# Optimization experiments

Measured on AMD Instinct MI355X. Metric: run time of the kernel, lower is better.

Reference implementation:

```python
import jax, jax.numpy as jnp
import numpy as np

N = 50000
E_RAND = 800000
IN_CH = 128
HID = 64
HEADS = 4
OUT_CH = 3
NEG_SLOPE = 0.2
BN_EPS = 1e-5


def setup_inputs() -> dict:
    key = jax.random.key(0)
    ks = jax.random.split(key, 24)
    x = jax.random.normal(ks[0], (N, IN_CH), dtype=jnp.float32)
    er = jax.random.randint(ks[1], (2, E_RAND), 0, N)
    sl = jnp.tile(jnp.arange(N, dtype=er.dtype)[None, :], (2, 1))
    edge_index = jnp.concatenate([er, sl], axis=1)  # [2, 850000]
    s = 0.1
    d1 = HID * HEADS            # 256
    d2 = (HID // 2) * HEADS     # 128
    inp = dict(x=x, edge_index=edge_index)
    # layer 1: in 128 -> heads*64
    inp["W1"] = s * jax.random.normal(ks[2], (IN_CH, HEADS * HID), dtype=jnp.float32)
    inp["a1s"] = s * jax.random.normal(ks[3], (HEADS, HID), dtype=jnp.float32)
    inp["a1d"] = s * jax.random.normal(ks[4], (HEADS, HID), dtype=jnp.float32)
    inp["b1"] = jnp.zeros((d1,), jnp.float32)
    inp["g1"] = jnp.ones((d1,), jnp.float32)
    inp["be1"] = jnp.zeros((d1,), jnp.float32)
    inp["m1"] = 0.01 * jax.random.normal(ks[5], (d1,), dtype=jnp.float32)
    inp["v1"] = jnp.ones((d1,), jnp.float32) + 0.01 * jax.random.uniform(ks[6], (d1,))
    # layer 2: in 256 -> heads*32
    inp["W2"] = s * jax.random.normal(ks[7], (d1, HEADS * (HID // 2)), dtype=jnp.float32)
    inp["a2s"] = s * jax.random.normal(ks[8], (HEADS, HID // 2), dtype=jnp.float32)
    inp["a2d"] = s * jax.random.normal(ks[9], (HEADS, HID // 2), dtype=jnp.float32)
    inp["b2"] = jnp.zeros((d2,), jnp.float32)
    inp["g2"] = jnp.ones((d2,), jnp.float32)
    inp["be2"] = jnp.zeros((d2,), jnp.float32)
    inp["m2"] = 0.01 * jax.random.normal(ks[10], (d2,), dtype=jnp.float32)
    inp["v2"] = jnp.ones((d2,), jnp.float32) + 0.01 * jax.random.uniform(ks[11], (d2,))
    # layer 3: in 128 -> 1 head, out_ch, concat=False
    inp["W3"] = s * jax.random.normal(ks[12], (d2, OUT_CH), dtype=jnp.float32)
    inp["a3s"] = s * jax.random.normal(ks[13], (1, OUT_CH), dtype=jnp.float32)
    inp["a3d"] = s * jax.random.normal(ks[14], (1, OUT_CH), dtype=jnp.float32)
    inp["b3"] = jnp.zeros((OUT_CH,), jnp.float32)
    return inp


def gat_conv(x, src, dst, W, a_src, a_dst, b, heads, fdim, concat):
    n = x.shape[0]
    h = (x @ W).reshape(n, heads, fdim)           # [N,H,F]
    als = jnp.einsum('nhf,hf->nh', h, a_src)      # [N,H]
    ald = jnp.einsum('nhf,hf->nh', h, a_dst)
    e = jax.nn.leaky_relu(als[src] + ald[dst], NEG_SLOPE)  # [E,H]
    m = jax.lax.stop_gradient(jax.ops.segment_max(e, dst, num_segments=n))
    ex = jnp.exp(e - m[dst])
    ssum = jax.ops.segment_sum(ex, dst, num_segments=n)
    alpha = ex / (ssum[dst] + 1e-16)              # segment softmax over in-edges
    msg = h[src] * alpha[:, :, None]              # [E,H,F]
    out = jax.ops.segment_sum(msg, dst, num_segments=n)  # [N,H,F]
    out = out.reshape(n, heads * fdim) if concat else out.mean(axis=1)
    return out + b


def batch_norm(x, gamma, beta, mean, var):
    return (x - mean) * jax.lax.rsqrt(var + BN_EPS) * gamma + beta


def reference(x, edge_index, W1, a1s, a1d, b1, g1, be1, m1, v1,
              W2, a2s, a2d, b2, g2, be2, m2, v2,
              W3, a3s, a3d, b3):
    src, dst = edge_index[0], edge_index[1]
    h = gat_conv(x, src, dst, W1, a1s, a1d, b1, HEADS, HID, True)
    h = jax.nn.elu(batch_norm(h, g1, be1, m1, v1))
    h = gat_conv(h, src, dst, W2, a2s, a2d, b2, HEADS, HID // 2, True)
    h = jax.nn.elu(batch_norm(h, g2, be2, m2, v2))
    h = gat_conv(h, src, dst, W3, a3s, a3d, b3, 1, OUT_CH, False)
    return jax.nn.log_softmax(h, axis=1)
```

## Files before the change

### kernel.cpp

```cpp
#include <hip/hip_runtime.h>


#define WSZ 64

typedef short short8 __attribute__((ext_vector_type(8)));
typedef float float4v __attribute__((ext_vector_type(4)));

__device__ inline unsigned short f2bf(float f) {
  unsigned u = __float_as_uint(f);
  u += 0x7FFFu + ((u >> 16) & 1u);
  return (unsigned short)(u >> 16);
}


__global__ __launch_bounds__(256) void hist_kernel(const int* __restrict__ dst, int E,
                                                   int* __restrict__ deg) {
  int e = blockIdx.x * 256 + threadIdx.x;
  if (e < E) atomicAdd(&deg[dst[e]], 1);
}

__global__ __launch_bounds__(256) void block_sums_kernel(const int* __restrict__ deg, int n,
                                                         int* __restrict__ bsum) {
  __shared__ int sh[256];
  int t = threadIdx.x;
  int base = blockIdx.x * 1024 + t * 4;
  int v = 0;
#pragma unroll
  for (int j = 0; j < 4; ++j) {
    int idx = base + j;
    if (idx < n) v += deg[idx];
  }
  sh[t] = v;
  __syncthreads();
  for (int off = 128; off >= 1; off >>= 1) {
    if (t < off) sh[t] += sh[t + off];
    __syncthreads();
  }
  if (t == 0) bsum[blockIdx.x] = sh[0];
}

__global__ void tiny_scan_kernel(int* bsum, int nb) {
  if (threadIdx.x == 0 && blockIdx.x == 0) {
    int run = 0;
    for (int i = 0; i < nb; ++i) {
      int v = bsum[i];
      bsum[i] = run;
      run += v;
    }
  }
}

__global__ __launch_bounds__(256) void scan_write_kernel(const int* __restrict__ deg, int n,
                                                         const int* __restrict__ bbase,
                                                         int* __restrict__ row_start,
                                                         int* __restrict__ cursor) {
  __shared__ int sh[256];
  int t = threadIdx.x;
  int base = blockIdx.x * 1024 + t * 4;
  int v[4];
  int s = 0;
#pragma unroll
  for (int j = 0; j < 4; ++j) {
    int idx = base + j;
    v[j] = (idx < n) ? deg[idx] : 0;
    s += v[j];
  }
  sh[t] = s;
  __syncthreads();
  for (int off = 1; off < 256; off <<= 1) {
    int x = (t >= off) ? sh[t - off] : 0;
    __syncthreads();
    sh[t] += x;
    __syncthreads();
  }
  int excl = sh[t] - s + bbase[blockIdx.x];
#pragma unroll
  for (int j = 0; j < 4; ++j) {
    int idx = base + j;
    if (idx < n) {
      row_start[idx] = excl;
      cursor[idx] = excl;
    }
    excl += v[j];
  }
  if (blockIdx.x == gridDim.x - 1 && t == 255) row_start[n] = excl;
}

__global__ __launch_bounds__(256) void scatter_kernel(const int* __restrict__ src,
                                                      const int* __restrict__ dst, int E,
                                                      int* __restrict__ cursor,
                                                      int* __restrict__ csr_src) {
  int e = blockIdx.x * 256 + threadIdx.x;
  if (e < E) {
    int d = dst[e];
    int p = atomicAdd(&cursor[d], 1);
    csr_src[p] = src[e];
  }
}


__global__ __launch_bounds__(256) void conv_bf16x4(const float* __restrict__ in,
                                                   unsigned short* __restrict__ out, int n4) {
  int i = blockIdx.x * 256 + threadIdx.x;
  if (i < n4) {
    float4 v = ((const float4*)in)[i];
    ushort4 u;
    u.x = f2bf(v.x); u.y = f2bf(v.y); u.z = f2bf(v.z); u.w = f2bf(v.w);
    ((ushort4*)out)[i] = u;
  }
}

__global__ __launch_bounds__(256) void conv_w1t_kernel(const float* __restrict__ W1,
                                                       unsigned short* __restrict__ W1t) {
  int idx = blockIdx.x * 256 + threadIdx.x;
  int n = idx >> 7, k = idx & 127;
  W1t[idx] = f2bf(W1[k * 256 + n]);
}

__global__ __launch_bounds__(256) void conv_w2t_kernel(const float* __restrict__ W2,
                                                       unsigned short* __restrict__ W2t) {
  int idx = blockIdx.x * 256 + threadIdx.x;
  int n = idx >> 8, p = idx & 255;
  int kl = (p & ~63) | ((p & 3) << 4) | ((p >> 2) & 15);
  W2t[idx] = f2bf(W2[kl * 128 + n]);
}


template <int K, int NTOT>
__global__ __launch_bounds__(256) void gemm_mfma2(
    const unsigned short* __restrict__ A,
    const unsigned short* __restrict__ Bt,
    const float* __restrict__ a_s, const float* __restrict__ a_d,
    unsigned short* __restrict__ hout,
    float* __restrict__ als, float* __restrict__ ald,
    int M) {
  constexpr int COLS = NTOT / 2;
  constexpr int CFW = COLS / 16;
  constexpr int HLOG = NTOT / 4;
  constexpr int CFH = HLOG / 16;
  constexpr int VPT = NTOT / 64;
  constexpr int KS = K / 32;
  __shared__ __align__(16) unsigned short Bs[COLS][K + 8];

  const int t = threadIdx.x;
  const int w = t >> 6;
  const int lane = t & 63;
  const int c16 = lane & 15;
  const int q = lane >> 4;
  const int gcol = blockIdx.y;
  const int bm = blockIdx.x * 128;

  {
    constexpr int TPR = K / 64;
    int nloc = t / TPR;
    int part = (t % TPR) * 64;
    const unsigned short* srcp = Bt + (size_t)(gcol * COLS + nloc) * K + part;
#pragma unroll
    for (int j = 0; j < 8; ++j) {
      uint4 v = *(const uint4*)(srcp + j * 8);
      *(uint4*)&Bs[nloc][part + j * 8] = v;
    }
  }
  int arow[2];
  arow[0] = min(bm + w * 32 + c16, M - 1);
  arow[1] = min(bm + w * 32 + 16 + c16, M - 1);
  short8 afr[2];
#pragma unroll
  for (int rf = 0; rf < 2; ++rf)
    afr[rf] = *(const short8*)(A + (size_t)arow[rf] * K + q * 8);
  __syncthreads();

  float4v acc[2][CFW];
#pragma unroll
  for (int rf = 0; rf < 2; ++rf)
#pragma unroll
    for (int cf = 0; cf < CFW; ++cf) acc[rf][cf] = float4v{0.f, 0.f, 0.f, 0.f};

#pragma unroll
  for (int ks = 0; ks < KS; ++ks) {
    short8 anx[2];
    if (ks + 1 < KS) {
#pragma unroll
      for (int rf = 0; rf < 2; ++rf)
        anx[rf] = *(const short8*)(A + (size_t)arow[rf] * K + (ks + 1) * 32 + q * 8);
    }
#pragma unroll
    for (int cf = 0; cf < CFW; ++cf) {
      short8 bfrag = *(const short8*)&Bs[cf * 16 + c16][ks * 32 + q * 8];
#pragma unroll
      for (int rf = 0; rf < 2; ++rf)
        acc[rf][cf] =
            __builtin_amdgcn_mfma_f32_16x16x32_bf16(afr[rf], bfrag, acc[rf][cf], 0, 0, 0);
    }
    if (ks + 1 < KS) {
      afr[0] = anx[0];
      afr[1] = anx[1];
    }
  }

  float sasv[CFW], sadv[CFW];
#pragma unroll
  for (int cf = 0; cf < CFW; ++cf) {
    int L = gcol * COLS + cf * 16 + c16;
    sasv[cf] = a_s[L];
    sadv[cf] = a_d[L];
  }
#pragma unroll
  for (int rf = 0; rf < 2; ++rf) {
#pragma unroll
    for (int r = 0; r < 4; ++r) {
      int n = bm + w * 32 + rf * 16 + q * 4 + r;
      float ps[2] = {0.f, 0.f}, pd[2] = {0.f, 0.f};
      unsigned short us[CFW];
#pragma unroll
      for (int cf = 0; cf < CFW; ++cf) {
        float v = acc[rf][cf][r];
        us[cf] = f2bf(v);
        ps[cf / CFH] += v * sasv[cf];
        pd[cf / CFH] += v * sadv[cf];
      }
#pragma unroll
      for (int off = 1; off <= 8; off <<= 1) {
#pragma unroll
        for (int hl = 0; hl < 2; ++hl) {
          ps[hl] += __shfl_xor(ps[hl], off, 16);
          pd[hl] += __shfl_xor(pd[hl], off, 16);
        }
      }
      if (n < M) {
#pragma unroll
        for (int hl = 0; hl < 2; ++hl) {
          int head = gcol * 2 + hl;
          unsigned short* dst = hout + (size_t)n * NTOT + head * HLOG + c16 * VPT;
          if constexpr (VPT == 4) {
            ushort4 u;
            u.x = us[hl * 4 + 0]; u.y = us[hl * 4 + 1];
            u.z = us[hl * 4 + 2]; u.w = us[hl * 4 + 3];
            *(ushort4*)dst = u;
          } else {
            ushort2 u;
            u.x = us[hl * 2 + 0]; u.y = us[hl * 2 + 1];
            *(ushort2*)dst = u;
          }
          if (c16 == 0) {
            als[(size_t)n * 4 + head] = ps[hl];
            ald[(size_t)n * 4 + head] = pd[hl];
          }
        }
      }
    }
  }
}


template <int D, bool FUSEL3>
__global__ __launch_bounds__(256) void gat_aggregate(
    const unsigned short* __restrict__ h_bf, const float* __restrict__ als,
    const float* __restrict__ ald, const int* __restrict__ row_start,
    const int* __restrict__ csr_src, const float* __restrict__ bias,
    const float* __restrict__ gamma, const float* __restrict__ beta,
    const float* __restrict__ bmean, const float* __restrict__ bvar,
    unsigned short* __restrict__ obf,
    const float* __restrict__ W3, const float* __restrict__ a3s,
    const float* __restrict__ a3d, float4* __restrict__ h3p,
    float* __restrict__ ald3,
    int n_nodes) {
  constexpr int VPT = D / WSZ;
  constexpr int H = 4;
  __shared__ float w3s[384];
  __shared__ float sa3[6];
  if constexpr (FUSEL3) {
    for (int i = threadIdx.x; i < 384; i += 256) w3s[i] = W3[i];
    if (threadIdx.x < 3) {
      sa3[threadIdx.x] = a3s[threadIdx.x];
      sa3[3 + threadIdx.x] = a3d[threadIdx.x];
    }
    __syncthreads();
  }
  int wid = threadIdx.x >> 6, lane = threadIdx.x & 63;
  int n = blockIdx.x * 4 + wid;
  if (n >= n_nodes) return;
  int c = lane * VPT;
  int hd = lane >> 4;
  float aldv = ald[(size_t)n * H + hd];
  int row = row_start[n], end = row_start[n + 1];
  float acc[VPT] = {};
  float ssum = 0.f;
  int i = row;

#define EDGE_BLOCK(B)                                                          \
  for (; i + (B) - 1 < end; i += (B)) {                                        \
    int s[B];                                                                  \
    float e[B];                                                                \
    _Pragma("unroll") for (int j = 0; j < (B); ++j) s[j] = csr_src[i + j];     \
    _Pragma("unroll") for (int j = 0; j < (B); ++j) e[j] =                     \
        als[(size_t)s[j] * H + hd] + aldv;                                     \
    if constexpr (VPT == 4) {                                                  \
      uint2 u[B];                                                              \
      _Pragma("unroll") for (int j = 0; j < (B); ++j) u[j] =                   \
          *(const uint2*)(h_bf + (size_t)s[j] * D + c);                        \
      _Pragma("unroll") for (int j = 0; j < (B); ++j) {                        \
        float ee = e[j];                                                       \
        ee = (ee > 0.f) ? ee : 0.2f * ee;                                      \
        float ex = __expf(ee);                                                 \
        ssum += ex;                                                            \
        acc[0] += ex * __uint_as_float(u[j].x << 16);                          \
        acc[1] += ex * __uint_as_float(u[j].x & 0xFFFF0000u);                  \
        acc[2] += ex * __uint_as_float(u[j].y << 16);                          \
        acc[3] += ex * __uint_as_float(u[j].y & 0xFFFF0000u);                  \
      }                                                                        \
    } else {                                                                   \
      unsigned u[B];                                                           \
      _Pragma("unroll") for (int j = 0; j < (B); ++j) u[j] =                   \
          *(const unsigned*)(h_bf + (size_t)s[j] * D + c);                     \
      _Pragma("unroll") for (int j = 0; j < (B); ++j) {                        \
        float ee = e[j];                                                       \
        ee = (ee > 0.f) ? ee : 0.2f * ee;                                      \
        float ex = __expf(ee);                                                 \
        ssum += ex;                                                            \
        acc[0] += ex * __uint_as_float(u[j] << 16);                            \
        acc[1] += ex * __uint_as_float(u[j] & 0xFFFF0000u);                    \
      }                                                                        \
    }                                                                          \
  }

  EDGE_BLOCK(8)
  EDGE_BLOCK(4)
  EDGE_BLOCK(1)
#undef EDGE_BLOCK

  float inv = 1.f / (ssum + 1e-16f);
#pragma unroll
  for (int j = 0; j < VPT; ++j) {
    int cl = hd * (VPT * 16) + j * 16 + (lane & 15);
    float o = acc[j] * inv + bias[cl];
    o = (o - bmean[cl]) * rsqrtf(bvar[cl] + 1e-5f) * gamma[cl] + beta[cl];
    o = (o > 0.f) ? o : (__expf(o) - 1.f);
    acc[j] = o;
  }
  if constexpr (!FUSEL3) {
    ushort4 u;
    u.x = f2bf(acc[0]); u.y = f2bf(acc[1]); u.z = f2bf(acc[2]); u.w = f2bf(acc[3]);
    *(ushort4*)(obf + (size_t)n * D + c) = u;
  } else {
    int k0l = hd * 32 + (lane & 15);
    int k1l = k0l + 16;
    float p0 = acc[0] * w3s[k0l * 3 + 0] + acc[1] * w3s[k1l * 3 + 0];
    float p1 = acc[0] * w3s[k0l * 3 + 1] + acc[1] * w3s[k1l * 3 + 1];
    float p2 = acc[0] * w3s[k0l * 3 + 2] + acc[1] * w3s[k1l * 3 + 2];
#pragma unroll
    for (int off = 32; off >= 1; off >>= 1) {
      p0 += __shfl_xor(p0, off, 64);
      p1 += __shfl_xor(p1, off, 64);
      p2 += __shfl_xor(p2, off, 64);
    }
    if (lane == 0) {
      float als3 = p0 * sa3[0] + p1 * sa3[1] + p2 * sa3[2];
      float ad3 = p0 * sa3[3] + p1 * sa3[4] + p2 * sa3[5];
      h3p[n] = make_float4(p0, p1, p2, als3);
      ald3[n] = ad3;
    }
  }
}


__global__ __launch_bounds__(256) void l3_agg_kernel(const float4* __restrict__ h3p,
                                                     const float* __restrict__ ald3,
                                                     const int* __restrict__ row_start,
                                                     const int* __restrict__ csr_src,
                                                     const float* __restrict__ b3,
                                                     float* __restrict__ out, int n_nodes) {
  int wid = threadIdx.x >> 6, lane = threadIdx.x & 63;
  int n = blockIdx.x * 4 + wid;
  if (n >= n_nodes) return;
  float aldv = ald3[n];
  int row = row_start[n], end = row_start[n + 1];
  float a0 = 0.f, a1 = 0.f, a2 = 0.f, ss = 0.f;
  for (int i = row + lane; i < end; i += 64) {
    int s = csr_src[i];
    float4 hv = h3p[s];
    float e = hv.w + aldv;
    e = (e > 0.f) ? e : 0.2f * e;
    float ex = __expf(e);
    ss += ex;
    a0 += ex * hv.x;
    a1 += ex * hv.y;
    a2 += ex * hv.z;
  }
#pragma unroll
  for (int off = 32; off >= 1; off >>= 1) {
    a0 += __shfl_xor(a0, off, 64);
    a1 += __shfl_xor(a1, off, 64);
    a2 += __shfl_xor(a2, off, 64);
    ss += __shfl_xor(ss, off, 64);
  }
  if (lane == 0) {
    float inv = 1.f / (ss + 1e-16f);
    float o0 = a0 * inv + b3[0];
    float o1 = a1 * inv + b3[1];
    float o2 = a2 * inv + b3[2];
    float m = fmaxf(o0, fmaxf(o1, o2));
    float lse = m + logf(expf(o0 - m) + expf(o1 - m) + expf(o2 - m));
    out[n * 3 + 0] = o0 - lse;
    out[n * 3 + 1] = o1 - lse;
    out[n * 3 + 2] = o2 - lse;
  }
}


extern "C" void kernel_launch(void* const* d_in, const int* in_sizes, int n_in,
                              void* d_out, int out_size, void* d_ws, size_t ws_size,
                              hipStream_t stream) {
  const float* x   = (const float*)d_in[0];
  const int*   ei  = (const int*)d_in[1];
  const float* W1  = (const float*)d_in[2];
  const float* a1s = (const float*)d_in[3];
  const float* a1d = (const float*)d_in[4];
  const float* b1  = (const float*)d_in[5];
  const float* g1v = (const float*)d_in[6];
  const float* be1 = (const float*)d_in[7];
  const float* m1  = (const float*)d_in[8];
  const float* v1  = (const float*)d_in[9];
  const float* W2  = (const float*)d_in[10];
  const float* a2s = (const float*)d_in[11];
  const float* a2d = (const float*)d_in[12];
  const float* b2  = (const float*)d_in[13];
  const float* g2v = (const float*)d_in[14];
  const float* be2 = (const float*)d_in[15];
  const float* m2  = (const float*)d_in[16];
  const float* v2  = (const float*)d_in[17];
  const float* W3  = (const float*)d_in[18];
  const float* a3s = (const float*)d_in[19];
  const float* a3d = (const float*)d_in[20];
  const float* b3  = (const float*)d_in[21];
  float* out = (float*)d_out;

  const int N = in_sizes[0] / 128;
  const int E = in_sizes[1] / 2;
  const int* srcv = ei;
  const int* dstv = ei + E;

  float* wsf  = (float*)d_ws;
  float* als1 = wsf;
  float* ald1 = als1 + (size_t)N * 4;
  float* als2 = ald1 + (size_t)N * 4;
  float* ald2 = als2 + (size_t)N * 4;
  float* h3p  = ald2 + (size_t)N * 4;
  float* ald3 = h3p + (size_t)N * 4;
  unsigned short* x_bf  = (unsigned short*)(ald3 + N);
  unsigned short* h_bf1 = x_bf + (size_t)N * 128;
  unsigned short* o1_bf = h_bf1 + (size_t)N * 256;
  unsigned short* h_bf2 = o1_bf + (size_t)N * 256;
  unsigned short* W1t   = h_bf2 + (size_t)N * 128;
  unsigned short* W2t   = W1t + 256 * 128;
  int* deg       = (int*)(W2t + 128 * 256);
  int* row_start = deg + N;
  int* cursor    = row_start + (N + 1);
  int* csr_src   = cursor + (N + 1);
  int* bsum      = csr_src + E;

  const int eb = (E + 255) / 256;
  const int nb = (N + 1023) / 1024;
  const int nodes4 = (N + 3) / 4;
  const dim3 gemm_grid((N + 127) / 128, 2);

  conv_bf16x4<<<(N * 128 / 4 + 255) / 256, 256, 0, stream>>>(x, x_bf, N * 128 / 4);
  conv_w1t_kernel<<<128, 256, 0, stream>>>(W1, W1t);
  conv_w2t_kernel<<<128, 256, 0, stream>>>(W2, W2t);

  hipMemsetAsync(deg, 0, (size_t)N * sizeof(int), stream);
  hist_kernel<<<eb, 256, 0, stream>>>(dstv, E, deg);
  block_sums_kernel<<<nb, 256, 0, stream>>>(deg, N, bsum);
  tiny_scan_kernel<<<1, 64, 0, stream>>>(bsum, nb);
  scan_write_kernel<<<nb, 256, 0, stream>>>(deg, N, bsum, row_start, cursor);
  scatter_kernel<<<eb, 256, 0, stream>>>(srcv, dstv, E, cursor, csr_src);

  gemm_mfma2<128, 256><<<gemm_grid, 256, 0, stream>>>(x_bf, W1t, a1s, a1d, h_bf1, als1,
                                                      ald1, N);
  gat_aggregate<256, false><<<nodes4, 256, 0, stream>>>(
      h_bf1, als1, ald1, row_start, csr_src, b1, g1v, be1, m1, v1, o1_bf, nullptr, nullptr,
      nullptr, nullptr, nullptr, N);
  gemm_mfma2<256, 128><<<gemm_grid, 256, 0, stream>>>(o1_bf, W2t, a2s, a2d, h_bf2, als2,
                                                      ald2, N);
  gat_aggregate<128, true><<<nodes4, 256, 0, stream>>>(
      h_bf2, als2, ald2, row_start, csr_src, b2, g2v, be2, m2, v2, nullptr, W3, a3s, a3d,
      (float4*)h3p, ald3, N);
  l3_agg_kernel<<<nodes4, 256, 0, stream>>>((const float4*)h3p, ald3, row_start, csr_src,
                                            b3, out, N);
}
```

Before: 388.8 us.

## Fuse fp32-to-bf16 input conversion into first GEMM and merge small prep kernels

The first GEMM now reads fp32 x directly and converts it to bf16 in registers, so the separate conversion kernel and its bf16 buffer are gone. The two weight-transpose kernels are merged into one launch, and the serial block-sum scan becomes a wavefront shuffle scan. The GEMM also preloads all A fragments for every K step up front instead of double-buffering, which raises register pressure. Together these are meant to cut launches and one full pass over x, at the cost of the GEMM reading fp32 data, twice the bytes per A element. The shuffle scan only handles up to 64 blocks, which holds for N=50000.

```diff
diff --git a/kernel.cpp b/kernel.cpp
--- a/kernel.cpp
+++ b/kernel.cpp
@@ -39,15 +39,16 @@
   if (t == 0) bsum[blockIdx.x] = sh[0];
 }
 
-__global__ void tiny_scan_kernel(int* bsum, int nb) {
-  if (threadIdx.x == 0 && blockIdx.x == 0) {
-    int run = 0;
-    for (int i = 0; i < nb; ++i) {
-      int v = bsum[i];
-      bsum[i] = run;
-      run += v;
-    }
-  }
+__global__ void scan_blocks_kernel(int* bsum, int nb) {
+  int lane = threadIdx.x & 63;
+  int orig = (lane < nb) ? bsum[lane] : 0;
+  int v = orig;
+#pragma unroll
+  for (int off = 1; off < 64; off <<= 1) {
+    int o = __shfl_up(v, off, 64);
+    if (lane >= off) v += o;
+  }
+  if (lane < nb) bsum[lane] = v - orig;
 }
 
 __global__ __launch_bounds__(256) void scan_write_kernel(const int* __restrict__ deg, int n,
@@ -98,37 +99,27 @@
   }
 }
 
-
-__global__ __launch_bounds__(256) void conv_bf16x4(const float* __restrict__ in,
-                                                   unsigned short* __restrict__ out, int n4) {
-  int i = blockIdx.x * 256 + threadIdx.x;
-  if (i < n4) {
-    float4 v = ((const float4*)in)[i];
-    ushort4 u;
-    u.x = f2bf(v.x); u.y = f2bf(v.y); u.z = f2bf(v.z); u.w = f2bf(v.w);
-    ((ushort4*)out)[i] = u;
-  }
-}
-
-__global__ __launch_bounds__(256) void conv_w1t_kernel(const float* __restrict__ W1,
-                                                       unsigned short* __restrict__ W1t) {
-  int idx = blockIdx.x * 256 + threadIdx.x;
-  int n = idx >> 7, k = idx & 127;
-  W1t[idx] = f2bf(W1[k * 256 + n]);
-}
-
-__global__ __launch_bounds__(256) void conv_w2t_kernel(const float* __restrict__ W2,
-                                                       unsigned short* __restrict__ W2t) {
-  int idx = blockIdx.x * 256 + threadIdx.x;
-  int n = idx >> 8, p = idx & 255;
-  int kl = (p & ~63) | ((p & 3) << 4) | ((p >> 2) & 15);
-  W2t[idx] = f2bf(W2[kl * 128 + n]);
-}
-
-
-template <int K, int NTOT>
+__global__ __launch_bounds__(256) void conv_weights_kernel(const float* __restrict__ W1,
+                                                           const float* __restrict__ W2,
+                                                           unsigned short* __restrict__ W1t,
+                                                           unsigned short* __restrict__ W2t) {
+  int b = blockIdx.x;
+  if (b < 128) {
+    int idx = b * 256 + threadIdx.x;
+    int n = idx >> 7, k = idx & 127;
+    W1t[idx] = f2bf(W1[k * 256 + n]);
+  } else {
+    int idx = (b - 128) * 256 + threadIdx.x;
+    int n = idx >> 8, p = idx & 255;
+    int kl = (p & ~63) | ((p & 3) << 4) | ((p >> 2) & 15);
+    W2t[idx] = f2bf(W2[kl * 128 + n]);
+  }
+}
+
+
+template <int K, int NTOT, bool AF32>
 __global__ __launch_bounds__(256) void gemm_mfma2(
-    const unsigned short* __restrict__ A,
+    const void* __restrict__ Ap,
     const unsigned short* __restrict__ Bt,
     const float* __restrict__ a_s, const float* __restrict__ a_d,
     unsigned short* __restrict__ hout,
@@ -161,40 +152,60 @@
       *(uint4*)&Bs[nloc][part + j * 8] = v;
     }
   }
+
   int arow[2];
   arow[0] = min(bm + w * 32 + c16, M - 1);
   arow[1] = min(bm + w * 32 + 16 + c16, M - 1);
-  short8 afr[2];
+  short8 afr[2][KS];
+  if constexpr (AF32) {
+    float4 fv[2][KS][2];
+#pragma unroll
+    for (int rf = 0; rf < 2; ++rf) {
+      const float* rp = (const float*)Ap + (size_t)arow[rf] * K;
+#pragma unroll
+      for (int ks = 0; ks < KS; ++ks) {
+        fv[rf][ks][0] = *(const float4*)(rp + ks * 32 + q * 8);
+        fv[rf][ks][1] = *(const float4*)(rp + ks * 32 + q * 8 + 4);
+      }
+    }
+#pragma unroll
+    for (int rf = 0; rf < 2; ++rf)
+#pragma unroll
+      for (int ks = 0; ks < KS; ++ks) {
+        ushort4 u0, u1;
+        u0.x = f2bf(fv[rf][ks][0].x); u0.y = f2bf(fv[rf][ks][0].y);
+        u0.z = f2bf(fv[rf][ks][0].z); u0.w = f2bf(fv[rf][ks][0].w);
+        u1.x = f2bf(fv[rf][ks][1].x); u1.y = f2bf(fv[rf][ks][1].y);
+        u1.z = f2bf(fv[rf][ks][1].z); u1.w = f2bf(fv[rf][ks][1].w);
+        union { ushort4 u[2]; short8 s; } cvt;
+        cvt.u[0] = u0; cvt.u[1] = u1;
+        afr[rf][ks] = cvt.s;
+      }
+  } else {
+    const unsigned short* Ab = (const unsigned short*)Ap;
+#pragma unroll
+    for (int rf = 0; rf < 2; ++rf)
+#pragma unroll
+      for (int ks = 0; ks < KS; ++ks)
+        afr[rf][ks] = *(const short8*)(Ab + (size_t)arow[rf] * K + ks * 32 + q * 8);
+  }
+  __syncthreads();
+
+  float4v acc[2][CFW];
 #pragma unroll
   for (int rf = 0; rf < 2; ++rf)
-    afr[rf] = *(const short8*)(A + (size_t)arow[rf] * K + q * 8);
-  __syncthreads();
-
-  float4v acc[2][CFW];
-#pragma unroll
-  for (int rf = 0; rf < 2; ++rf)
 #pragma unroll
     for (int cf = 0; cf < CFW; ++cf) acc[rf][cf] = float4v{0.f, 0.f, 0.f, 0.f};
 
 #pragma unroll
   for (int ks = 0; ks < KS; ++ks) {
-    short8 anx[2];
-    if (ks + 1 < KS) {
-#pragma unroll
-      for (int rf = 0; rf < 2; ++rf)
-        anx[rf] = *(const short8*)(A + (size_t)arow[rf] * K + (ks + 1) * 32 + q * 8);
-    }
 #pragma unroll
     for (int cf = 0; cf < CFW; ++cf) {
       short8 bfrag = *(const short8*)&Bs[cf * 16 + c16][ks * 32 + q * 8];
 #pragma unroll
       for (int rf = 0; rf < 2; ++rf)
         acc[rf][cf] =
-            __builtin_amdgcn_mfma_f32_16x16x32_bf16(afr[rf], bfrag, acc[rf][cf], 0, 0, 0);
-    }
-    if (ks + 1 < KS) {
-      afr[0] = anx[0];
-      afr[1] = anx[1];
+            __builtin_amdgcn_mfma_f32_16x16x32_bf16(afr[rf][ks], bfrag, acc[rf][cf], 0, 0, 0);
     }
   }
 
@@ -447,8 +458,7 @@
   float* ald2 = als2 + (size_t)N * 4;
   float* h3p  = ald2 + (size_t)N * 4;
   float* ald3 = h3p + (size_t)N * 4;
-  unsigned short* x_bf  = (unsigned short*)(ald3 + N);
-  unsigned short* h_bf1 = x_bf + (size_t)N * 128;
+  unsigned short* h_bf1 = (unsigned short*)(ald3 + N);
   unsigned short* o1_bf = h_bf1 + (size_t)N * 256;
   unsigned short* h_bf2 = o1_bf + (size_t)N * 256;
   unsigned short* W1t   = h_bf2 + (size_t)N * 128;
@@ -464,24 +474,22 @@
   const int nodes4 = (N + 3) / 4;
   const dim3 gemm_grid((N + 127) / 128, 2);
 
-  conv_bf16x4<<<(N * 128 / 4 + 255) / 256, 256, 0, stream>>>(x, x_bf, N * 128 / 4);
-  conv_w1t_kernel<<<128, 256, 0, stream>>>(W1, W1t);
-  conv_w2t_kernel<<<128, 256, 0, stream>>>(W2, W2t);
+  conv_weights_kernel<<<256, 256, 0, stream>>>(W1, W2, W1t, W2t);
 
   hipMemsetAsync(deg, 0, (size_t)N * sizeof(int), stream);
   hist_kernel<<<eb, 256, 0, stream>>>(dstv, E, deg);
   block_sums_kernel<<<nb, 256, 0, stream>>>(deg, N, bsum);
-  tiny_scan_kernel<<<1, 64, 0, stream>>>(bsum, nb);
+  scan_blocks_kernel<<<1, 64, 0, stream>>>(bsum, nb);
   scan_write_kernel<<<nb, 256, 0, stream>>>(deg, N, bsum, row_start, cursor);
   scatter_kernel<<<eb, 256, 0, stream>>>(srcv, dstv, E, cursor, csr_src);
 
-  gemm_mfma2<128, 256><<<gemm_grid, 256, 0, stream>>>(x_bf, W1t, a1s, a1d, h_bf1, als1,
-                                                      ald1, N);
+  gemm_mfma2<128, 256, true><<<gemm_grid, 256, 0, stream>>>(x, W1t, a1s, a1d, h_bf1, als1,
+                                                            ald1, N);
   gat_aggregate<256, false><<<nodes4, 256, 0, stream>>>(
       h_bf1, als1, ald1, row_start, csr_src, b1, g1v, be1, m1, v1, o1_bf, nullptr, nullptr,
       nullptr, nullptr, nullptr, N);
-  gemm_mfma2<256, 128><<<gemm_grid, 256, 0, stream>>>(o1_bf, W2t, a2s, a2d, h_bf2, als2,
-                                                      ald2, N);
+  gemm_mfma2<256, 128, false><<<gemm_grid, 256, 0, stream>>>(o1_bf, W2t, a2s, a2d, h_bf2,
+                                                             als2, ald2, N);
   gat_aggregate<128, true><<<nodes4, 256, 0, stream>>>(
       h_bf2, als2, ald2, row_start, csr_src, b2, g2v, be2, m2, v2, nullptr, W3, a3s, a3d,
       (float4*)h3p, ald3, N);
```

Result: no change. 383.6 us (-1.3%).
